# Performance work log

Hardware: AMD Instinct MI355X
Metric: run time of the kernel (lower is better)

Reference implementation:

```python
import math
import jax, jax.numpy as jnp
import numpy as np

C = 1.0          # Poincare ball curvature
NUM_HEADS = 8
EPS = 1e-15

def _beta(a, b):
    # Beta function via lgamma (python float constant)
    return math.exp(math.lgamma(a) + math.lgamma(b) - math.lgamma(a + b))

def h_linear(x, z, r, c=C):
    """HNN++ Poincare fully-connected layer (hypll HLinear).
    x: [..., in] points in the ball; z: [in, out] tangent weights; r: [out] bias."""
    sc = math.sqrt(c)
    x2 = jnp.sum(x * x, axis=-1, keepdims=True)
    lam = 2.0 / (1.0 - c * x2)                                # conformal factor
    zn = jnp.maximum(jnp.linalg.norm(z, axis=0), EPS)          # [out]
    inner = x @ z                                              # [..., out]
    two_scr = 2.0 * sc * r
    d = (2.0 * zn / sc) * jnp.arcsinh(
        (sc * inner * lam / zn) * jnp.cosh(two_scr) - (lam - 1.0) * jnp.sinh(two_scr)
    )
    w = jnp.sinh(sc * d) / sc
    return w / (1.0 + jnp.sqrt(1.0 + c * jnp.sum(w * w, axis=-1, keepdims=True)))

def pairwise_dist(q, k, c=C):
    """Poincare distance d(q,k) = arccosh(1 + 2c|q-k|^2 / ((1-c|q|^2)(1-c|k|^2))) / sqrt(c).
    q,k: [B,H,S,hd] -> [B,H,S,S]."""
    q2 = jnp.sum(q * q, axis=-1)
    k2 = jnp.sum(k * k, axis=-1)
    qk = jnp.einsum('bhqd,bhkd->bhqk', q, k)
    diff2 = jnp.maximum(q2[..., :, None] + k2[..., None, :] - 2.0 * qk, 0.0)
    denom = (1.0 - c * q2)[..., :, None] * (1.0 - c * k2)[..., None, :]
    arg = 1.0 + 2.0 * c * diff2 / denom
    return jnp.arccosh(jnp.maximum(arg, 1.0 + 1e-7)) / math.sqrt(c)

def midpoint(v, w, c=C):
    """Weighted Mobius gyromidpoint: m = 1/2 (x) (sum w*lam*x / sum w*(lam-1)).
    v: [B,H,Sk,hd], w: [B,H,Sq,Sk] -> [B,H,Sq,hd]."""
    v2 = jnp.sum(v * v, axis=-1)                      # [B,H,Sk]
    lam = 2.0 / (1.0 - c * v2)
    num = jnp.einsum('bhqk,bhkd->bhqd', w * lam[..., None, :], v)
    den = jnp.maximum(jnp.einsum('bhqk,bhk->bhq', w, lam - 1.0), EPS)[..., None]
    g = num / den                                     # gyromidpoint pre-scaling
    sc = math.sqrt(c)
    gn = jnp.maximum(jnp.linalg.norm(g, axis=-1, keepdims=True), EPS)
    t = jnp.tanh(0.5 * jnp.arctanh(jnp.clip(sc * gn, 0.0, 1.0 - 1e-7)))
    return (t / sc) * g / gn

def _forward(query, key, value, Wq, bq, Wk, bk, Wv, bv, scale_tau, scale_gamma):
    B, S, E = query.shape
    H = NUM_HEADS
    hd = E // H
    # hyperbolic q/k/v projections, then split into heads: [B,H,S,hd]
    q = h_linear(query, Wq, bq).reshape(B, S, H, hd).transpose(0, 2, 1, 3)
    k = h_linear(key, Wk, bk).reshape(B, S, H, hd).transpose(0, 2, 1, 3)
    v = h_linear(value, Wv, bv).reshape(B, S, H, hd).transpose(0, 2, 1, 3)
    # similarity = -dist/tau - gamma with tau = exp(-scale_tau)
    sim = -pairwise_dist(q, k) * jnp.exp(scale_tau[0]) - scale_gamma[0]
    causal = jnp.triu(jnp.ones((S, S), dtype=bool), k=1)
    sim = jnp.where(causal, -jnp.inf, sim)
    w = jnp.exp(sim)                                  # 'exp' attention activation
    agg = midpoint(v, w)                              # [B,H,S,hd]
    agg = agg.transpose(0, 2, 1, 3).reshape(B, S, E)
    # HNN++ beta-concatenation of the per-head ball points
    scale = _beta(E / 2.0, 0.5) / _beta(hd / 2.0, 0.5)
    return agg * scale

def setup_inputs() -> dict:
    root = jax.random.key(0)
    ks = jax.random.split(root, 8)
    B, S, E = 1, 2048, 512
    s = 0.02  # keep points well inside the unit ball
    return {
        'query': s * jax.random.normal(ks[0], (B, S, E), jnp.float32),
        'key':   s * jax.random.normal(ks[1], (B, S, E), jnp.float32),
        'value': s * jax.random.normal(ks[2], (B, S, E), jnp.float32),
        'Wq': s * jax.random.normal(ks[3], (E, E), jnp.float32),
        'Wk': s * jax.random.normal(ks[4], (E, E), jnp.float32),
        'Wv': s * jax.random.normal(ks[5], (E, E), jnp.float32),
        'bq': jnp.zeros((E,), jnp.float32),
        'bk': jnp.zeros((E,), jnp.float32),
        'bv': jnp.zeros((E,), jnp.float32),
        'scale_tau': jnp.zeros((1,), jnp.float32),
        'scale_gamma': jnp.zeros((1,), jnp.float32),
    }

def reference(query, key, value, Wq, Wk, Wv, bq, bk, bv, scale_tau, scale_gamma):
    return _forward(query, key, value, Wq, bq, Wk, bk, Wv, bv, scale_tau, scale_gamma)
```

## Files before the change

kernel.cpp:

```cpp
#include <hip/hip_runtime.h>
#include <cmath>

#define H 8
#define SEQ 2048
#define EDIM 512
#define HD 64
#define EPSF 1e-15f

typedef short bf16x8 __attribute__((ext_vector_type(8)));
typedef float f32x4 __attribute__((ext_vector_type(4)));

#define ZN_OFF    16
#define STATS_OFF (ZN_OFF + 24 * EDIM)
#define CQ_OFF    (STATS_OFF + 3 * H * SEQ)
#define IK_OFF    (CQ_OFF + H * SEQ)
#define PX2_OFF   (IK_OFF + H * SEQ)
#define U16_OFF   (PX2_OFF + 12288 + 16)
#define WT_U16    0
#define QKVB_U16  (WT_U16 + 3 * EDIM * EDIM)
#define VT_U16    (QKVB_U16 + 3 * SEQ * EDIM)
#define U16_TOTAL (VT_U16 + H * 80 * SEQ)
#define BIG_OFF   (U16_OFF + U16_TOTAL / 2 + 16)
#define TRI_SLOTS 272
#define PART_U16S (H * TRI_SLOTS * 4 * 1280)
#define ACC_FLOATS  (H * SEQ * 80)

__device__ __forceinline__ float bf2f(unsigned short u){
  union { unsigned int i; float f; } v; v.i = ((unsigned int)u) << 16; return v.f;
}
__device__ __forceinline__ unsigned short f2bf(float f){
  union { float f; unsigned int i; } v; v.f = f;
  unsigned int x = v.i;
  unsigned int r = (x + 0x7fffu + ((x >> 16) & 1u)) >> 16;
  return (unsigned short)r;
}

__device__ __forceinline__ unsigned int cvt_pk_bf16(float a, float b){
  unsigned int r;
  asm("v_cvt_pk_bf16_f32 %0, %1, %2" : "=v"(r) : "v"(a), "v"(b));
  return r;
}
__device__ __forceinline__ float vlog2f(float x){
  float r; asm("v_log_f32 %0, %1" : "=v"(r) : "v"(x)); return r;
}
__device__ __forceinline__ float vexp2f(float x){
  float r; asm("v_exp_f32 %0, %1" : "=v"(r) : "v"(x)); return r;
}
__device__ __forceinline__ float vsqrtf(float x){
  float r; asm("v_sqrt_f32 %0, %1" : "=v"(r) : "v"(x)); return r;
}

__device__ __forceinline__ int detect_f32(const unsigned short* __restrict__ q){
  const int l = threadIdx.x & 63;
  float mx = 0.f;
  #pragma unroll
  for (int j = 0; j < 4; ++j) mx = fmaxf(mx, fabsf(bf2f(q[l * 4 + j])));
  #pragma unroll
  for (int m = 32; m >= 1; m >>= 1) mx = fmaxf(mx, __shfl_xor(mx, m, 64));
  return mx > 1000.f;
}

__device__ __forceinline__ int tri_base(int t){
  const int m = t >> 1;
  return (t & 1) ? (m + 1) * (m + 1) : m * (m + 1);
}

__global__ __launch_bounds__(256) void wcvt_kernel(
    const void* __restrict__ Wq, const void* __restrict__ Wk, const void* __restrict__ Wv,
    const unsigned short* __restrict__ qprobe,
    unsigned short* __restrict__ WT, float* __restrict__ zn)
{
  const int p = blockIdx.y;
  const int bi = blockIdx.x >> 3, bo = blockIdx.x & 7;
  const void* W = (p == 0) ? Wq : ((p == 1) ? Wk : Wv);
  const int t = threadIdx.x;
  const int isf32 = detect_f32(qprobe);
  __shared__ float tile[64][65];

  #pragma unroll
  for (int j = 0; j < 16; ++j){
    int idx = t + 256 * j;
    int il = idx >> 6, ol = idx & 63;
    float val;
    if (isf32) val = ((const float*)W)[(size_t)(bi * 64 + il) * EDIM + bo * 64 + ol];
    else       val = bf2f(((const unsigned short*)W)[(size_t)(bi * 64 + il) * EDIM + bo * 64 + ol]);
    tile[il][ol] = val;
  }
  __syncthreads();
  if (t < 64){
    float s = 0.f;
    #pragma unroll 8
    for (int i = 0; i < 64; ++i){ float v = tile[i][t]; s += v * v; }
    zn[((size_t)(bi * 3 + p)) * EDIM + bo * 64 + t] = s;
  }
  #pragma unroll
  for (int j = 0; j < 16; ++j){
    int idx = t + 256 * j;
    int ol = idx >> 6, il = idx & 63;
    WT[((size_t)p * EDIM + bo * 64 + ol) * EDIM + bi * 64 + il] = f2bf(tile[il][ol]);
  }
}

__global__ __launch_bounds__(256) void hlin_gemm_kernel(
    const void* __restrict__ Xq, const void* __restrict__ Xk, const void* __restrict__ Xv,
    const unsigned short* __restrict__ WT, const unsigned short* __restrict__ qprobe,
    unsigned short* __restrict__ partC, float* __restrict__ partX2)
{
  const int p = blockIdx.y;
  const int rg = blockIdx.x >> 1;
  const int kslice = blockIdx.x & 1;
  const void* X = (p == 0) ? Xq : ((p == 1) ? Xk : Xv);
  const int r0 = rg * 16;
  const int t  = threadIdx.x;
  const int w = t >> 6, lane = t & 63;
  const int col = lane & 15, quad = lane >> 4;
  const int isf32 = detect_f32(qprobe);
  const int koff = kslice * 256;

  const unsigned short* WTb = WT + ((size_t)p * EDIM + w * 128 + col) * EDIM + koff;
  const float* Xf = (const float*)X + (size_t)(r0 + col) * EDIM + koff;
  const unsigned short* Xh = (const unsigned short*)X + (size_t)(r0 + col) * EDIM + koff;

  f32x4 acc[8];
  #pragma unroll
  for (int nt = 0; nt < 8; ++nt) acc[nt] = (f32x4){0.f, 0.f, 0.f, 0.f};
  float x2part = 0.f;

  bf16x8 caf, naf;
  bf16x8 cbf[8], nbf[8];
  {
    if (isf32){
      float4 xa = *(const float4*)&Xf[quad * 8];
      float4 xb = *(const float4*)&Xf[quad * 8 + 4];
      float xv[8] = {xa.x, xa.y, xa.z, xa.w, xb.x, xb.y, xb.z, xb.w};
      #pragma unroll
      for (int j = 0; j < 8; ++j){ caf[j] = (short)f2bf(xv[j]); x2part += xv[j] * xv[j]; }
    } else {
      caf = *(const bf16x8*)&Xh[quad * 8];
      #pragma unroll
      for (int j = 0; j < 8; ++j){ float xv = bf2f((unsigned short)caf[j]); x2part += xv * xv; }
    }
    #pragma unroll
    for (int nt = 0; nt < 8; ++nt)
      cbf[nt] = *(const bf16x8*)&WTb[(size_t)nt * 16 * EDIM + quad * 8];
  }

  for (int ks = 0; ks < 8; ++ks){
// ... 64 lines not shown
  for (int nt = 0; nt < 8; ++nt)
    #pragma unroll
    for (int r = 0; r < 4; ++r){
      const size_t idx = (size_t)(quad * 4 + r) * 512 + w * 128 + nt * 16 + col;
      acc[nt][r] = bf2f(partC[base0 + idx]) + bf2f(partC[base1 + idx]);
    }

  float lamr[4], lm1[4];
  #pragma unroll
  for (int r = 0; r < 4; ++r){
    const int row = quad * 4 + r;
    float x2r = partX2[((size_t)(p * 128 + rg) * 2 + 0) * 16 + row] +
                partX2[((size_t)(p * 128 + rg) * 2 + 1) * 16 + row];
    lamr[r] = 2.f / (1.f - x2r);
    lm1[r] = lamr[r] - 1.f;
  }
  #pragma unroll
  for (int nt = 0; nt < 8; ++nt){
    const int n = w * 128 + nt * 16 + col;
    float zsum = 0.f;
    #pragma unroll
    for (int bi = 0; bi < 8; ++bi)
      zsum += znacc[((size_t)(bi * 3 + p)) * EDIM + n];
    float znv = fmaxf(sqrtf(zsum), EPSF);
    float rb;
    if (isf32) rb = ((const float*)Bb)[n];
    else       rb = bf2f(((const unsigned short*)Bb)[n]);
    float e2r = __expf(2.f * rb);
    float ie2r = 1.f / e2r;
    float ch = 0.5f * (e2r + ie2r), sh = 0.5f * (e2r - ie2r);
    float izn = 1.f / znv;
    float tz = 2.f * znv;
    #pragma unroll
    for (int r = 0; r < 4; ++r){
      float a = (acc[nt][r] * lamr[r] * izn) * ch - lm1[r] * sh;
      float b = a + sqrtf(a * a + 1.f);
      float tt = __expf(tz * __logf(b));
      smem[(quad * 4 + r) * EDIM + n] = 0.5f * (tt - 1.f / tt);
    }
  }
  __syncthreads();

  {
    int row = t >> 4, l = t & 15;
    float s = 0.f;
    for (int o = l; o < EDIM; o += 16){ float wv = smem[row * EDIM + o]; s += wv * wv; }
    #pragma unroll
    for (int m = 8; m >= 1; m >>= 1) s += __shfl_xor(s, m, 16);
    if (l == 0) sw2[row] = s;
  }
  __syncthreads();

  const int o0 = 2 * t;
  const int h0 = t >> 5;
  const int d0 = o0 & 63;
  const int l5 = t & 31;
  #pragma unroll
  for (int rr = 0; rr < 16; ++rr){
    float inv = 1.f / (1.f + sqrtf(1.f + sw2[rr]));
    unsigned short b0 = f2bf(smem[rr * EDIM + o0] * inv);
    unsigned short b1 = f2bf(smem[rr * EDIM + o0 + 1] * inv);
    float r0v = bf2f(b0), r1v = bf2f(b1);
    int s = r0 + rr;
    unsigned int* dst = (unsigned int*)&qkvb[(((size_t)p * H + h0) * SEQ + s) * HD + d0];
    *dst = (unsigned int)b0 | ((unsigned int)b1 << 16);
    float ss = r0v * r0v + r1v * r1v;
    #pragma unroll
    for (int m = 16; m >= 1; m >>= 1) ss += __shfl_xor(ss, m, 64);
    if (p == 2){
      float lam = 2.f / (1.f - ss);
      VT[((size_t)h0 * 80 + d0) * SEQ + s]     = f2bf(r0v * lam);
      VT[((size_t)h0 * 80 + d0 + 1) * SEQ + s] = f2bf(r1v * lam);
      if (l5 < 16)
        VT[((size_t)h0 * 80 + 64 + l5) * SEQ + s] = (l5 == 0) ? f2bf(lam - 1.f) : 0;
    }
    if (l5 == 0){
      stats[((size_t)p * H + h0) * SEQ + s] = ss;
      if (p == 0) cqs[(size_t)h0 * SEQ + s] = 2.f / (1.f - ss);
      if (p == 1) iks[(size_t)h0 * SEQ + s] = 1.f / (1.f - ss);
    }
  }
}

__global__ __launch_bounds__(64) void attn_kernel(
    const unsigned short* __restrict__ Qb, const unsigned short* __restrict__ Kb,
    const unsigned short* __restrict__ VT,
    const float* __restrict__ q2s_all, const float* __restrict__ k2s_all,
    const float* __restrict__ cqs_all, const float* __restrict__ iks_all,
    const void* __restrict__ tau, const void* __restrict__ gam,
    const unsigned short* __restrict__ qprobe,
    float* __restrict__ big, int use_part)
{
  const int h  = blockIdx.y;
  const int tile = 31 - (blockIdx.x >> 5);
  const int sl = (blockIdx.x >> 1) & 15;
  const int wp = blockIdx.x & 1;
  const int kBeg = sl * 128;
  const int kEndFull = (tile + 1) * 64;
  if (kBeg >= kEndFull) return;
  const int kEnd = (kBeg + 128 < kEndFull) ? (kBeg + 128) : kEndFull;
  const int nhalf = (kEnd - kBeg) >> 5;

  const int lane = threadIdx.x;
  const int col = lane & 15, quad = lane >> 4;
  const int q0A = tile * 64 + wp * 16;
  const int q0B = q0A + 32;

  const unsigned short* Qh  = Qb + (size_t)h * SEQ * HD;
  const unsigned short* Kh  = Kb + (size_t)h * SEQ * HD;
  const unsigned short* VTh = VT + (size_t)h * 80 * SEQ;
  const float* q2s = q2s_all + (size_t)h * SEQ;
  const float* k2s = k2s_all + (size_t)h * SEQ;
  const float* cqs = cqs_all + (size_t)h * SEQ;
  const float* iks = iks_all + (size_t)h * SEQ;

  const int isf32 = detect_f32(qprobe);
  float tauv, gamv;
  if (isf32){ tauv = ((const float*)tau)[0]; gamv = ((const float*)gam)[0]; }
  else      { tauv = bf2f(((const unsigned short*)tau)[0]);
              gamv = bf2f(((const unsigned short*)gam)[0]); }
  const float m_et = -__expf(tauv);
  const float m_g2 = -gamv * 1.44269504088896340736f;

  const int srcA = ((quad & 1) * 2) * 16 + col;
  const int srcB = srcA + 16;
  const int tsel = quad >> 1;

  bf16x8 qfA0 = *(const bf16x8*)&Qh[(size_t)(q0A + col) * HD + quad * 8];
  bf16x8 qfA1 = *(const bf16x8*)&Qh[(size_t)(q0A + col) * HD + 32 + quad * 8];
  bf16x8 qfB0 = *(const bf16x8*)&Qh[(size_t)(q0B + col) * HD + quad * 8];
  bf16x8 qfB1 = *(const bf16x8*)&Qh[(size_t)(q0B + col) * HD + 32 + quad * 8];
  const float q2A = q2s[q0A + col], q2B = q2s[q0B + col];
  const float cqA = cqs[q0A + col], cqB = cqs[q0B + col];
  const int qmaxA = q0A + col, qmaxB = q0B + col;

  f32x4 pvA[5], pvB[5];
  #pragma unroll
  for (int nt = 0; nt < 5; ++nt){
    pvA[nt] = (f32x4){0.f, 0.f, 0.f, 0.f};
    pvB[nt] = (f32x4){0.f, 0.f, 0.f, 0.f};
  }

  int kb32 = kBeg;

  bf16x8 ckf0[2], ckf1[2], nkf0[2], nkf1[2];
  float4 ck2[2], cik[2], nk2[2], nik[2];
  #pragma unroll
  for (int tt = 0; tt < 2; ++tt){
    const int kbase = kb32 + 16 * tt;
    ckf0[tt] = *(const bf16x8*)&Kh[(size_t)(kbase + col) * HD + quad * 8];
    ckf1[tt] = *(const bf16x8*)&Kh[(size_t)(kbase + col) * HD + 32 + quad * 8];
    ck2[tt]  = *(const float4*)&k2s[kbase + quad * 4];
    cik[tt]  = *(const float4*)&iks[kbase + quad * 4];
  }

  for (int i = 0; i < nhalf; ++i){
    const int nkb32 = kb32 + 32;
    const bool have_next = (i + 1 < nhalf);
    if (have_next){
      #pragma unroll
      for (int tt = 0; tt < 2; ++tt){
        const int kbase = nkb32 + 16 * tt;
        nkf0[tt] = *(const bf16x8*)&Kh[(size_t)(kbase + col) * HD + quad * 8];
        nkf1[tt] = *(const bf16x8*)&Kh[(size_t)(kbase + col) * HD + 32 + quad * 8];
        nk2[tt]  = *(const float4*)&k2s[kbase + quad * 4];
        nik[tt]  = *(const float4*)&iks[kbase + quad * 4];
      }
    }

    unsigned int tloA[2], thiA[2], tloB[2], thiB[2];
    #pragma unroll
    for (int tt = 0; tt < 2; ++tt){
      const int kbase = kb32 + 16 * tt;
      f32x4 sA = (f32x4){0.f, 0.f, 0.f, 0.f};
      f32x4 sB = (f32x4){0.f, 0.f, 0.f, 0.f};
      sA = __builtin_amdgcn_mfma_f32_16x16x32_bf16(ckf0[tt], qfA0, sA, 0, 0, 0);
      sB = __builtin_amdgcn_mfma_f32_16x16x32_bf16(ckf0[tt], qfB0, sB, 0, 0, 0);
      sA = __builtin_amdgcn_mfma_f32_16x16x32_bf16(ckf1[tt], qfA1, sA, 0, 0, 0);
      sB = __builtin_amdgcn_mfma_f32_16x16x32_bf16(ckf1[tt], qfB1, sB, 0, 0, 0);
      float wA[4], wB[4];
      #pragma unroll
      for (int r = 0; r < 4; ++r){
        float k2 = (r == 0) ? ck2[tt].x : (r == 1) ? ck2[tt].y : (r == 2) ? ck2[tt].z : ck2[tt].w;
        float ik = (r == 0) ? cik[tt].x : (r == 1) ? cik[tt].y : (r == 2) ? cik[tt].z : cik[tt].w;
        const int key = kbase + quad * 4 + r;
        {
          float diff2 = fmaxf(q2A + k2 - 2.f * sA[r], 0.f);
          float u = fmaxf(diff2 * cqA * ik, 1e-7f);
          float z = 1.f + u + vsqrtf(u * (u + 2.f));
          float wv = vexp2f(__builtin_fmaf(vlog2f(z), m_et, m_g2));
          wA[r] = (key > qmaxA) ? 0.f : wv;
        }
        {
          float diff2 = fmaxf(q2B + k2 - 2.f * sB[r], 0.f);
          float u = fmaxf(diff2 * cqB * ik, 1e-7f);
          float z = 1.f + u + vsqrtf(u * (u + 2.f));
          float wv = vexp2f(__builtin_fmaf(vlog2f(z), m_et, m_g2));
          wB[r] = (key > qmaxB) ? 0.f : wv;
        }
      }
      tloA[tt] = cvt_pk_bf16(wA[0], wA[1]);
      thiA[tt] = cvt_pk_bf16(wA[2], wA[3]);
      tloB[tt] = cvt_pk_bf16(wB[0], wB[1]);
      thiB[tt] = cvt_pk_bf16(wB[2], wB[3]);
    }
    union { uint4 u; bf16x8 v; } pwA, pwB;
    {
      unsigned int a0 = (unsigned int)__shfl((int)tloA[0], srcA, 64);
      unsigned int a1 = (unsigned int)__shfl((int)tloA[1], srcA, 64);
      unsigned int b0 = (unsigned int)__shfl((int)thiA[0], srcA, 64);
      unsigned int b1 = (unsigned int)__shfl((int)thiA[1], srcA, 64);
      unsigned int c0 = (unsigned int)__shfl((int)tloA[0], srcB, 64);
      unsigned int c1 = (unsigned int)__shfl((int)tloA[1], srcB, 64);
      unsigned int d0 = (unsigned int)__shfl((int)thiA[0], srcB, 64);
      unsigned int d1 = (unsigned int)__shfl((int)thiA[1], srcB, 64);
      pwA.u.x = tsel ? a1 : a0;
      pwA.u.y = tsel ? b1 : b0;
      pwA.u.z = tsel ? c1 : c0;
      pwA.u.w = tsel ? d1 : d0;
    }
    {
      unsigned int a0 = (unsigned int)__shfl((int)tloB[0], srcA, 64);
      unsigned int a1 = (unsigned int)__shfl((int)tloB[1], srcA, 64);
      unsigned int b0 = (unsigned int)__shfl((int)thiB[0], srcA, 64);
      unsigned int b1 = (unsigned int)__shfl((int)thiB[1], srcA, 64);
      unsigned int c0 = (unsigned int)__shfl((int)tloB[0], srcB, 64);
      unsigned int c1 = (unsigned int)__shfl((int)tloB[1], srcB, 64);
      unsigned int d0 = (unsigned int)__shfl((int)thiB[0], srcB, 64);
      unsigned int d1 = (unsigned int)__shfl((int)thiB[1], srcB, 64);
      pwB.u.x = tsel ? a1 : a0;
      pwB.u.y = tsel ? b1 : b0;
      pwB.u.z = tsel ? c1 : c0;
      pwB.u.w = tsel ? d1 : d0;
    }
    #pragma unroll
    for (int nt = 0; nt < 5; ++nt){
      bf16x8 vf = *(const bf16x8*)&VTh[(size_t)(16 * nt + col) * SEQ + kb32 + quad * 8];
      pvA[nt] = __builtin_amdgcn_mfma_f32_16x16x32_bf16(pwA.v, vf, pvA[nt], 0, 0, 0);
      pvB[nt] = __builtin_amdgcn_mfma_f32_16x16x32_bf16(pwB.v, vf, pvB[nt], 0, 0, 0);
    }

    if (have_next){
      #pragma unroll
      for (int tt = 0; tt < 2; ++tt){
        ckf0[tt] = nkf0[tt]; ckf1[tt] = nkf1[tt];
        ck2[tt] = nk2[tt];   cik[tt] = nik[tt];
      }
    }
    kb32 = nkb32;
  }

  if (use_part){
    const int tbase = tri_base(tile);
    uint2* slotA = (uint2*)big + (size_t)(((h * TRI_SLOTS + tbase + sl) * 4) + wp) * 320;
    uint2* slotB = (uint2*)big + (size_t)(((h * TRI_SLOTS + tbase + sl) * 4) + wp + 2) * 320;
    #pragma unroll
    for (int nt = 0; nt < 5; ++nt){
      uint2 pk;
      pk.x = cvt_pk_bf16(pvA[nt][0], pvA[nt][1]);
      pk.y = cvt_pk_bf16(pvA[nt][2], pvA[nt][3]);
      slotA[nt * 64 + lane] = pk;
      pk.x = cvt_pk_bf16(pvB[nt][0], pvB[nt][1]);
      pk.y = cvt_pk_bf16(pvB[nt][2], pvB[nt][3]);
      slotB[nt * 64 + lane] = pk;
    }
  } else {
    #pragma unroll
    for (int r = 0; r < 4; ++r){
      float* rowA = big + ((size_t)h * SEQ + q0A + quad * 4 + r) * 80;
      float* rowB = big + ((size_t)h * SEQ + q0B + quad * 4 + r) * 80;
      #pragma unroll
      for (int nt = 0; nt < 5; ++nt){
        atomicAdd(&rowA[16 * nt + col], pvA[nt][r]);
        atomicAdd(&rowB[16 * nt + col], pvB[nt][r]);
      }
    }
  }
}

__global__ __launch_bounds__(256) void attn_fin_kernel(
    const float* __restrict__ big, int use_part,
    float* __restrict__ out, float beta_scale)
{
  const int h = blockIdx.y, tile16 = blockIdx.x;
  const int t = threadIdx.x;
  const int w = t >> 6, lane = t & 63;
  const int col = lane & 15, quad = lane >> 4;
  const int q0 = tile16 * 16;

  __shared__ float red[4][64][20];

  f32x4 pv[5];
  #pragma unroll
  for (int nt = 0; nt < 5; ++nt) pv[nt] = (f32x4){0.f, 0.f, 0.f, 0.f};

  if (use_part){
    const int st = tile16 >> 2, wq = tile16 & 3;
    const int tbase = tri_base(st);
    const int nv = (st + 2) >> 1;
    for (int sl = w; sl < nv; sl += 4){
      const uint2* slot = (const uint2*)big +
          (size_t)((h * TRI_SLOTS + tbase + sl) * 4 + wq) * 320;
      #pragma unroll
      for (int nt = 0; nt < 5; ++nt){
        uint2 v = slot[nt * 64 + lane];
        pv[nt][0] += bf2f((unsigned short)(v.x & 0xffffu));
        pv[nt][1] += bf2f((unsigned short)(v.x >> 16));
        pv[nt][2] += bf2f((unsigned short)(v.y & 0xffffu));
        pv[nt][3] += bf2f((unsigned short)(v.y >> 16));
      }
    }
  } else if (w == 0){
    #pragma unroll
    for (int nt = 0; nt < 5; ++nt)
      #pragma unroll
      for (int r = 0; r < 4; ++r)
        pv[nt][r] = big[((size_t)h * SEQ + q0 + quad * 4 + r) * 80 + 16 * nt + col];
  }

  #pragma unroll
  for (int nt = 0; nt < 5; ++nt)
    *(float4*)&red[w][lane][nt * 4] = (float4){pv[nt][0], pv[nt][1], pv[nt][2], pv[nt][3]};
  __syncthreads();

  if (t < 64){
    #pragma unroll
    for (int nt = 0; nt < 5; ++nt){
      float4 a = *(const float4*)&red[0][t][nt * 4];
      float4 b = *(const float4*)&red[1][t][nt * 4];
      float4 c = *(const float4*)&red[2][t][nt * 4];
      float4 d = *(const float4*)&red[3][t][nt * 4];
      pv[nt][0] = a.x + b.x + c.x + d.x;
      pv[nt][1] = a.y + b.y + c.y + d.y;
      pv[nt][2] = a.z + b.z + c.z + d.z;
      pv[nt][3] = a.w + b.w + c.w + d.w;
    }
    #pragma unroll
    for (int r = 0; r < 4; ++r){
      float den = __shfl(pv[4][r], quad * 16, 64);
      den = fmaxf(den, EPSF);
      float inv_den = 1.f / den;
      float g[4];
      float gsq = 0.f;
      #pragma unroll
      for (int nt = 0; nt < 4; ++nt){ g[nt] = pv[nt][r] * inv_den; gsq += g[nt] * g[nt]; }
      #pragma unroll
      for (int m = 8; m >= 1; m >>= 1) gsq += __shfl_xor(gsq, m, 64);
      float gn = fmaxf(sqrtf(gsq), EPSF);
      float x = fminf(gn, 1.f - 1e-7f);
      float tt2 = x / (1.f + sqrtf(1.f - x * x));
      float scl = (tt2 / gn) * beta_scale;
      const int q = q0 + quad * 4 + r;
      #pragma unroll
      for (int nt = 0; nt < 4; ++nt)
        out[(size_t)q * EDIM + h * HD + 16 * nt + col] = g[nt] * scl;
    }
  }
}

extern "C" void kernel_launch(void* const* d_in, const int* in_sizes, int n_in,
                              void* d_out, int out_size, void* d_ws, size_t ws_size,
                              hipStream_t stream){
  const void* Xq  = d_in[0];
  const void* Xk  = d_in[1];
  const void* Xv  = d_in[2];
  const void* Wq  = d_in[3];
  const void* Wk  = d_in[4];
  const void* Wv  = d_in[5];
  const void* Bq  = d_in[6];
  const void* Bk  = d_in[7];
  const void* Bv  = d_in[8];
  const void* tau = d_in[9];
  const void* gam = d_in[10];

  float* wsf   = (float*)d_ws;
  float* zn    = wsf + ZN_OFF;
  float* stats = wsf + STATS_OFF;
  float* cqs   = wsf + CQ_OFF;
  float* iks   = wsf + IK_OFF;
  float* px2   = wsf + PX2_OFF;
  unsigned short* u16b = (unsigned short*)(wsf + U16_OFF);
  unsigned short* WT   = u16b + WT_U16;
  unsigned short* qkvb = u16b + QKVB_U16;
  unsigned short* VT   = u16b + VT_U16;
  float* big   = wsf + BIG_OFF;
  unsigned short* partC = (unsigned short*)big;

  const int use_part =
      (ws_size >= (size_t)BIG_OFF * sizeof(float) + (size_t)PART_U16S * 2) ? 1 : 0;

  unsigned short* Qb = qkvb;
  unsigned short* Kb = qkvb + (size_t)H * SEQ * HD;
  float* q2s = stats;
  float* k2s = stats + (size_t)H * SEQ;
  const unsigned short* qprobe = (const unsigned short*)Xq;

  double lb1 = lgamma(EDIM / 2.0) + lgamma(0.5) - lgamma(EDIM / 2.0 + 0.5);
  double lb2 = lgamma(HD / 2.0)   + lgamma(0.5) - lgamma(HD / 2.0 + 0.5);
  float beta_scale = (float)exp(lb1 - lb2);

  wcvt_kernel<<<dim3(64, 3), dim3(256), 0, stream>>>(Wq, Wk, Wv, qprobe, WT, zn);
  hlin_gemm_kernel<<<dim3(256, 3), dim3(256), 0, stream>>>(
      Xq, Xk, Xv, WT, qprobe, partC, px2);
  hlin_fin_kernel<<<dim3(128, 3), dim3(256), 0, stream>>>(
      partC, px2, Bq, Bk, Bv, zn, qprobe, qkvb, stats, cqs, iks, VT);
  if (!use_part)
    hipMemsetAsync(big, 0, (size_t)ACC_FLOATS * sizeof(float), stream);
  attn_kernel<<<dim3(32 * 16 * 2, H), dim3(64), 0, stream>>>(
      Qb, Kb, VT, q2s, k2s, cqs, iks, tau, gam, qprobe, big, use_part);
  attn_fin_kernel<<<dim3(128, H), dim3(256), 0, stream>>>(
      big, use_part, (float*)d_out, beta_scale);
}
```

Measured before the change: 195.0 us.

## Pack four attention waves per block, template-unroll key loop, hoist V loads

```diff
diff --git a/kernel.cpp b/kernel.cpp
--- a/kernel.cpp
+++ b/kernel.cpp
@@ -293,66 +293,19 @@
   }
 }
 
-__global__ __launch_bounds__(64) void attn_kernel(
-    const unsigned short* __restrict__ Qb, const unsigned short* __restrict__ Kb,
-    const unsigned short* __restrict__ VT,
-    const float* __restrict__ q2s_all, const float* __restrict__ k2s_all,
-    const float* __restrict__ cqs_all, const float* __restrict__ iks_all,
-    const void* __restrict__ tau, const void* __restrict__ gam,
-    const unsigned short* __restrict__ qprobe,
-    float* __restrict__ big, int use_part)
+template<int NH>
+__device__ __forceinline__ void attn_loop(
+    int kb32, int col, int quad,
+    const unsigned short* __restrict__ Kh, const unsigned short* __restrict__ VTh,
+    const float* __restrict__ k2s, const float* __restrict__ iks,
+    bf16x8 qfA0, bf16x8 qfA1, bf16x8 qfB0, bf16x8 qfB1,
+    float cqA, float cqq2A, float cqB, float cqq2B,
+    int qmaxA, int qmaxB, float m_et, float m_g2,
+    int srcA, int srcB, int tsel,
+    f32x4 (&pvA)[5], f32x4 (&pvB)[5])
 {
-  const int h  = blockIdx.y;
-  const int tile = 31 - (blockIdx.x >> 5);
-  const int sl = (blockIdx.x >> 1) & 15;
-  const int wp = blockIdx.x & 1;
-  const int kBeg = sl * 128;
-  const int kEndFull = (tile + 1) * 64;
-  if (kBeg >= kEndFull) return;
-  const int kEnd = (kBeg + 128 < kEndFull) ? (kBeg + 128) : kEndFull;
-  const int nhalf = (kEnd - kBeg) >> 5;
-
-  const int lane = threadIdx.x;
-  const int col = lane & 15, quad = lane >> 4;
-  const int q0A = tile * 64 + wp * 16;
-  const int q0B = q0A + 32;
-
-  const unsigned short* Qh  = Qb + (size_t)h * SEQ * HD;
-  const unsigned short* Kh  = Kb + (size_t)h * SEQ * HD;
-  const unsigned short* VTh = VT + (size_t)h * 80 * SEQ;
-  const float* q2s = q2s_all + (size_t)h * SEQ;
-  const float* k2s = k2s_all + (size_t)h * SEQ;
-  const float* cqs = cqs_all + (size_t)h * SEQ;
-  const float* iks = iks_all + (size_t)h * SEQ;
-
-  const int isf32 = detect_f32(qprobe);
-  float tauv, gamv;
-  if (isf32){ tauv = ((const float*)tau)[0]; gamv = ((const float*)gam)[0]; }
-  else      { tauv = bf2f(((const unsigned short*)tau)[0]);
-              gamv = bf2f(((const unsigned short*)gam)[0]); }
-  const float m_et = -__expf(tauv);
-  const float m_g2 = -gamv * 1.44269504088896340736f;
-
-  const int srcA = ((quad & 1) * 2) * 16 + col;
-  const int srcB = srcA + 16;
-  const int tsel = quad >> 1;
-
-  bf16x8 qfA0 = *(const bf16x8*)&Qh[(size_t)(q0A + col) * HD + quad * 8];
-  bf16x8 qfA1 = *(const bf16x8*)&Qh[(size_t)(q0A + col) * HD + 32 + quad * 8];
-  bf16x8 qfB0 = *(const bf16x8*)&Qh[(size_t)(q0B + col) * HD + quad * 8];
-  bf16x8 qfB1 = *(const bf16x8*)&Qh[(size_t)(q0B + col) * HD + 32 + quad * 8];
-  const float q2A = q2s[q0A + col], q2B = q2s[q0B + col];
-  const float cqA = cqs[q0A + col], cqB = cqs[q0B + col];
-  const int qmaxA = q0A + col, qmaxB = q0B + col;
-
-  f32x4 pvA[5], pvB[5];
-  #pragma unroll
-  for (int nt = 0; nt < 5; ++nt){
-    pvA[nt] = (f32x4){0.f, 0.f, 0.f, 0.f};
-    pvB[nt] = (f32x4){0.f, 0.f, 0.f, 0.f};
-  }
-
-  int kb32 = kBeg;
+  const float m2cqA = -2.f * cqA;
+  const float m2cqB = -2.f * cqB;
 
   bf16x8 ckf0[2], ckf1[2], nkf0[2], nkf1[2];
   float4 ck2[2], cik[2], nk2[2], nik[2];
@@ -365,13 +318,17 @@
     cik[tt]  = *(const float4*)&iks[kbase + quad * 4];
   }
 
-  for (int i = 0; i < nhalf; ++i){
-    const int nkb32 = kb32 + 32;
-    const bool have_next = (i + 1 < nhalf);
-    if (have_next){
+  #pragma unroll
+  for (int i = 0; i < NH; ++i){
+    bf16x8 vf[5];
+    #pragma unroll
+    for (int nt = 0; nt < 5; ++nt)
+      vf[nt] = *(const bf16x8*)&VTh[(size_t)(16 * nt + col) * SEQ + kb32 + quad * 8];
+
+    if (i + 1 < NH){
       #pragma unroll
       for (int tt = 0; tt < 2; ++tt){
-        const int kbase = nkb32 + 16 * tt;
+        const int kbase = kb32 + 32 + 16 * tt;
         nkf0[tt] = *(const bf16x8*)&Kh[(size_t)(kbase + col) * HD + quad * 8];
         nkf1[tt] = *(const bf16x8*)&Kh[(size_t)(kbase + col) * HD + 32 + quad * 8];
         nk2[tt]  = *(const float4*)&k2s[kbase + quad * 4];
@@ -382,29 +339,32 @@
     unsigned int tloA[2], thiA[2], tloB[2], thiB[2];
     #pragma unroll
     for (int tt = 0; tt < 2; ++tt){
-      const int kbase = kb32 + 16 * tt;
       f32x4 sA = (f32x4){0.f, 0.f, 0.f, 0.f};
       f32x4 sB = (f32x4){0.f, 0.f, 0.f, 0.f};
+      __builtin_amdgcn_s_setprio(1);
       sA = __builtin_amdgcn_mfma_f32_16x16x32_bf16(ckf0[tt], qfA0, sA, 0, 0, 0);
       sB = __builtin_amdgcn_mfma_f32_16x16x32_bf16(ckf0[tt], qfB0, sB, 0, 0, 0);
       sA = __builtin_amdgcn_mfma_f32_16x16x32_bf16(ckf1[tt], qfA1, sA, 0, 0, 0);
       sB = __builtin_amdgcn_mfma_f32_16x16x32_bf16(ckf1[tt], qfB1, sB, 0, 0, 0);
+      __builtin_amdgcn_s_setprio(0);
       float wA[4], wB[4];
       #pragma unroll
       for (int r = 0; r < 4; ++r){
         float k2 = (r == 0) ? ck2[tt].x : (r == 1) ? ck2[tt].y : (r == 2) ? ck2[tt].z : ck2[tt].w;
         float ik = (r == 0) ? cik[tt].x : (r == 1) ? cik[tt].y : (r == 2) ? cik[tt].z : cik[tt].w;
-        const int key = kbase + quad * 4 + r;
+        const int key = kb32 + 16 * tt + quad * 4 + r;
         {
-          float diff2 = fmaxf(q2A + k2 - 2.f * sA[r], 0.f);
-          float u = fmaxf(diff2 * cqA * ik, 1e-7f);
+          float t1 = __builtin_fmaf(k2, cqA, cqq2A);
+          t1 = __builtin_fmaf(m2cqA, sA[r], t1);
+          float u = fmaxf(t1 * ik, 1e-7f);
           float z = 1.f + u + vsqrtf(u * (u + 2.f));
           float wv = vexp2f(__builtin_fmaf(vlog2f(z), m_et, m_g2));
           wA[r] = (key > qmaxA) ? 0.f : wv;
         }
         {
-          float diff2 = fmaxf(q2B + k2 - 2.f * sB[r], 0.f);
-          float u = fmaxf(diff2 * cqB * ik, 1e-7f);
+          float t1 = __builtin_fmaf(k2, cqB, cqq2B);
+          t1 = __builtin_fmaf(m2cqB, sB[r], t1);
+          float u = fmaxf(t1 * ik, 1e-7f);
           float z = 1.f + u + vsqrtf(u * (u + 2.f));
           float wv = vexp2f(__builtin_fmaf(vlog2f(z), m_et, m_g2));
           wB[r] = (key > qmaxB) ? 0.f : wv;
@@ -444,22 +404,94 @@
       pwB.u.z = tsel ? c1 : c0;
       pwB.u.w = tsel ? d1 : d0;
     }
+    __builtin_amdgcn_s_setprio(1);
     #pragma unroll
     for (int nt = 0; nt < 5; ++nt){
-      bf16x8 vf = *(const bf16x8*)&VTh[(size_t)(16 * nt + col) * SEQ + kb32 + quad * 8];
-      pvA[nt] = __builtin_amdgcn_mfma_f32_16x16x32_bf16(pwA.v, vf, pvA[nt], 0, 0, 0);
-      pvB[nt] = __builtin_amdgcn_mfma_f32_16x16x32_bf16(pwB.v, vf, pvB[nt], 0, 0, 0);
-    }
-
-    if (have_next){
+      pvA[nt] = __builtin_amdgcn_mfma_f32_16x16x32_bf16(pwA.v, vf[nt], pvA[nt], 0, 0, 0);
+      pvB[nt] = __builtin_amdgcn_mfma_f32_16x16x32_bf16(pwB.v, vf[nt], pvB[nt], 0, 0, 0);
+    }
+    __builtin_amdgcn_s_setprio(0);
+
+    if (i + 1 < NH){
       #pragma unroll
       for (int tt = 0; tt < 2; ++tt){
         ckf0[tt] = nkf0[tt]; ckf1[tt] = nkf1[tt];
         ck2[tt] = nk2[tt];   cik[tt] = nik[tt];
       }
     }
-    kb32 = nkb32;
-  }
+    kb32 += 32;
+  }
+}
+
+__global__ __launch_bounds__(256) void attn_kernel(
+    const unsigned short* __restrict__ Qb, const unsigned short* __restrict__ Kb,
+    const unsigned short* __restrict__ VT,
+    const float* __restrict__ q2s_all, const float* __restrict__ k2s_all,
+    const float* __restrict__ cqs_all, const float* __restrict__ iks_all,
+    const void* __restrict__ tau, const void* __restrict__ gam,
+    const unsigned short* __restrict__ qprobe,
+    float* __restrict__ big, int use_part)
+{
+  const int h  = blockIdx.y;
+  const int unit = blockIdx.x * 4 + (threadIdx.x >> 6);
+  const int lane = threadIdx.x & 63;
+  const int tile = 31 - (unit >> 5);
+  const int sl = (unit >> 1) & 15;
+  const int wp = unit & 1;
+  const int kBeg = sl * 128;
+  const int kEndFull = (tile + 1) * 64;
+  if (kBeg >= kEndFull) return;
+  const int kEnd = (kBeg + 128 < kEndFull) ? (kBeg + 128) : kEndFull;
+  const int nhalf = (kEnd - kBeg) >> 5;
+
+  const int col = lane & 15, quad = lane >> 4;
+  const int q0A = tile * 64 + wp * 16;
+  const int q0B = q0A + 32;
+
+  const unsigned short* Qh  = Qb + (size_t)h * SEQ * HD;
+  const unsigned short* Kh  = Kb + (size_t)h * SEQ * HD;
+  const unsigned short* VTh = VT + (size_t)h * 80 * SEQ;
+  const float* q2s = q2s_all + (size_t)h * SEQ;
+  const float* k2s = k2s_all + (size_t)h * SEQ;
+  const float* cqs = cqs_all + (size_t)h * SEQ;
+  const float* iks = iks_all + (size_t)h * SEQ;
+
+  const int isf32 = detect_f32(qprobe);
+  float tauv, gamv;
+  if (isf32){ tauv = ((const float*)tau)[0]; gamv = ((const float*)gam)[0]; }
+  else      { tauv = bf2f(((const unsigned short*)tau)[0]);
+              gamv = bf2f(((const unsigned short*)gam)[0]); }
+  const float m_et = -__expf(tauv);
+  const float m_g2 = -gamv * 1.44269504088896340736f;
+
+  const int srcA = ((quad & 1) * 2) * 16 + col;
+  const int srcB = srcA + 16;
+  const int tsel = quad >> 1;
+
+  bf16x8 qfA0 = *(const bf16x8*)&Qh[(size_t)(q0A + col) * HD + quad * 8];
+  bf16x8 qfA1 = *(const bf16x8*)&Qh[(size_t)(q0A + col) * HD + 32 + quad * 8];
+  bf16x8 qfB0 = *(const bf16x8*)&Qh[(size_t)(q0B + col) * HD + quad * 8];
+  bf16x8 qfB1 = *(const bf16x8*)&Qh[(size_t)(q0B + col) * HD + 32 + quad * 8];
+  const float q2A = q2s[q0A + col], q2B = q2s[q0B + col];
+  const float cqA = cqs[q0A + col], cqB = cqs[q0B + col];
+  const float cqq2A = cqA * q2A, cqq2B = cqB * q2B;
+  const int qmaxA = q0A + col, qmaxB = q0B + col;
+
+  f32x4 pvA[5], pvB[5];
+  #pragma unroll
+  for (int nt = 0; nt < 5; ++nt){
+    pvA[nt] = (f32x4){0.f, 0.f, 0.f, 0.f};
+    pvB[nt] = (f32x4){0.f, 0.f, 0.f, 0.f};
+  }
+
+  if (nhalf == 4)
+    attn_loop<4>(kBeg, col, quad, Kh, VTh, k2s, iks, qfA0, qfA1, qfB0, qfB1,
+                 cqA, cqq2A, cqB, cqq2B, qmaxA, qmaxB, m_et, m_g2,
+                 srcA, srcB, tsel, pvA, pvB);
+  else
+    attn_loop<2>(kBeg, col, quad, Kh, VTh, k2s, iks, qfA0, qfA1, qfB0, qfB1,
+                 cqA, cqq2A, cqB, cqq2B, qmaxA, qmaxB, m_et, m_g2,
+                 srcA, srcB, tsel, pvA, pvB);
 
   if (use_part){
     const int tbase = tri_base(tile);
@@ -617,7 +649,7 @@
       partC, px2, Bq, Bk, Bv, zn, qprobe, qkvb, stats, cqs, iks, VT);
   if (!use_part)
     hipMemsetAsync(big, 0, (size_t)ACC_FLOATS * sizeof(float), stream);
-  attn_kernel<<<dim3(32 * 16 * 2, H), dim3(64), 0, stream>>>(
+  attn_kernel<<<dim3(256, H), dim3(256), 0, stream>>>(
       Qb, Kb, VT, q2s, k2s, cqs, iks, tau, gam, qprobe, big, use_part);
   attn_fin_kernel<<<dim3(128, H), dim3(256), 0, stream>>>(
       big, use_part, (float*)d_out, beta_scale);
```

Result: no change. 195.1 us (+0.1%).

## Make attention key-stationary: hold a 64-key block in registers, loop over queries

Applied to the files above, without the earlier changes.

```diff
diff --git a/kernel.cpp b/kernel.cpp
--- a/kernel.cpp
+++ b/kernel.cpp
@@ -21,8 +21,8 @@
 #define VT_U16    (QKVB_U16 + 3 * SEQ * EDIM)
 #define U16_TOTAL (VT_U16 + H * 80 * SEQ)
 #define BIG_OFF   (U16_OFF + U16_TOTAL / 2 + 16)
-#define TRI_SLOTS 272
-#define PART_U16S (H * TRI_SLOTS * 4 * 1280)
+#define TRI16 2112
+#define PART_U16S (H * TRI16 * 1280)
 #define ACC_FLOATS  (H * SEQ * 80)
 
 __device__ __forceinline__ float bf2f(unsigned short u){
@@ -60,9 +60,9 @@
   return mx > 1000.f;
 }
 
-__device__ __forceinline__ int tri_base(int t){
-  const int m = t >> 1;
-  return (t & 1) ? (m + 1) * (m + 1) : m * (m + 1);
+__device__ __forceinline__ int sbase(int s){
+  const int a = s >> 2, b = s & 3;
+  return s + 2 * a * (a - 1) + a * b;
 }
 
 __global__ __launch_bounds__(256) void wcvt_kernel(
@@ -293,7 +293,157 @@
   }
 }
 
-__global__ __launch_bounds__(64) void attn_kernel(
+__device__ __forceinline__ uint4 xpose32(unsigned int tlo0, unsigned int tlo1,
+                                         unsigned int thi0, unsigned int thi1,
+                                         int srcA, int srcB, int tsel){
+  unsigned int a0 = (unsigned int)__shfl((int)tlo0, srcA, 64);
+  unsigned int a1 = (unsigned int)__shfl((int)tlo1, srcA, 64);
+  unsigned int b0 = (unsigned int)__shfl((int)thi0, srcA, 64);
+  unsigned int b1 = (unsigned int)__shfl((int)thi1, srcA, 64);
+  unsigned int c0 = (unsigned int)__shfl((int)tlo0, srcB, 64);
+  unsigned int c1 = (unsigned int)__shfl((int)tlo1, srcB, 64);
+  unsigned int d0 = (unsigned int)__shfl((int)thi0, srcB, 64);
+  unsigned int d1 = (unsigned int)__shfl((int)thi1, srcB, 64);
+  uint4 r;
+  r.x = tsel ? a1 : a0;
+  r.y = tsel ? b1 : b0;
+  r.z = tsel ? c1 : c0;
+  r.w = tsel ? d1 : d0;
+  return r;
+}
+
+__device__ __forceinline__ void score4(
+    const f32x4& s4, const float4& k2v, const float4& ikv,
+    float cq, float cqq2, float m2cq, int kbase, int qmax, int quad,
+    float m_et, float m_g2, unsigned int& lo, unsigned int& hi)
+{
+  float w[4];
+  #pragma unroll
+  for (int r = 0; r < 4; ++r){
+    float k2 = (r == 0) ? k2v.x : (r == 1) ? k2v.y : (r == 2) ? k2v.z : k2v.w;
+    float ik = (r == 0) ? ikv.x : (r == 1) ? ikv.y : (r == 2) ? ikv.z : ikv.w;
+    float t1 = __builtin_fmaf(k2, cq, cqq2);
+    t1 = __builtin_fmaf(m2cq, s4[r], t1);
+    float u = fmaxf(t1 * ik, 1e-7f);
+    float z = 1.f + u + vsqrtf(u * (u + 2.f));
+    float wv = vexp2f(__builtin_fmaf(vlog2f(z), m_et, m_g2));
+    const int key = kbase + quad * 4 + r;
+    w[r] = (key > qmax) ? 0.f : wv;
+  }
+  lo = cvt_pk_bf16(w[0], w[1]);
+  hi = cvt_pk_bf16(w[2], w[3]);
+}
+
+template<int NITER>
+__device__ __forceinline__ void attn_qloop(
+    int s0, int c, int kBeg, int col, int quad, int lane,
+    const unsigned short* __restrict__ Qh,
+    const bf16x8 (&kf0)[4], const bf16x8 (&kf1)[4],
+    const float4 (&ck2)[4], const float4 (&cik)[4],
+    const bf16x8 (&vf0)[5], const bf16x8 (&vf1)[5],
+    const float* __restrict__ q2s, const float* __restrict__ cqs,
+    float m_et, float m_g2, int srcA, int srcB, int tsel,
+    float* __restrict__ big, int h, int use_part)
+{
+  bf16x8 qA0 = *(const bf16x8*)&Qh[(size_t)(s0 * 16 + col) * HD + quad * 8];
+  bf16x8 qA1 = *(const bf16x8*)&Qh[(size_t)(s0 * 16 + col) * HD + 32 + quad * 8];
+  bf16x8 qB0 = *(const bf16x8*)&Qh[(size_t)((s0 + 1) * 16 + col) * HD + quad * 8];
+  bf16x8 qB1 = *(const bf16x8*)&Qh[(size_t)((s0 + 1) * 16 + col) * HD + 32 + quad * 8];
+  float q2A = q2s[s0 * 16 + col],       cqA = cqs[s0 * 16 + col];
+  float q2B = q2s[(s0 + 1) * 16 + col], cqB = cqs[(s0 + 1) * 16 + col];
+
+  #pragma unroll
+  for (int i = 0; i < NITER; ++i){
+    const int sA = s0 + 2 * i, sB = sA + 1;
+    bf16x8 nA0, nA1, nB0, nB1;
+    float nq2A, ncqA, nq2B, ncqB;
+    if (i + 1 < NITER){
+      const int tA = (sA + 2) * 16 + col, tB = (sA + 3) * 16 + col;
+      nA0 = *(const bf16x8*)&Qh[(size_t)tA * HD + quad * 8];
+      nA1 = *(const bf16x8*)&Qh[(size_t)tA * HD + 32 + quad * 8];
+      nB0 = *(const bf16x8*)&Qh[(size_t)tB * HD + quad * 8];
+      nB1 = *(const bf16x8*)&Qh[(size_t)tB * HD + 32 + quad * 8];
+      nq2A = q2s[tA]; ncqA = cqs[tA];
+      nq2B = q2s[tB]; ncqB = cqs[tB];
+    }
+
+    const float cqq2A = cqA * q2A, m2cqA = -2.f * cqA;
+    const float cqq2B = cqB * q2B, m2cqB = -2.f * cqB;
+    const int qmaxA = sA * 16 + col, qmaxB = sB * 16 + col;
+
+    f32x4 sSA[4], sSB[4];
+    __builtin_amdgcn_s_setprio(1);
+    #pragma unroll
+    for (int g = 0; g < 4; ++g){
+      f32x4 z4 = (f32x4){0.f, 0.f, 0.f, 0.f};
+      sSA[g] = __builtin_amdgcn_mfma_f32_16x16x32_bf16(kf0[g], qA0, z4, 0, 0, 0);
+      sSA[g] = __builtin_amdgcn_mfma_f32_16x16x32_bf16(kf1[g], qA1, sSA[g], 0, 0, 0);
+      sSB[g] = __builtin_amdgcn_mfma_f32_16x16x32_bf16(kf0[g], qB0, z4, 0, 0, 0);
+      sSB[g] = __builtin_amdgcn_mfma_f32_16x16x32_bf16(kf1[g], qB1, sSB[g], 0, 0, 0);
+    }
+    __builtin_amdgcn_s_setprio(0);
+
+    unsigned int loA[4], hiA[4], loB[4], hiB[4];
+    #pragma unroll
+    for (int g = 0; g < 4; ++g){
+      score4(sSA[g], ck2[g], cik[g], cqA, cqq2A, m2cqA, kBeg + g * 16, qmaxA, quad,
+             m_et, m_g2, loA[g], hiA[g]);
+      score4(sSB[g], ck2[g], cik[g], cqB, cqq2B, m2cqB, kBeg + g * 16, qmaxB, quad,
+             m_et, m_g2, loB[g], hiB[g]);
+    }
+
+    union { uint4 u; bf16x8 v; } pA01, pA23, pB01, pB23;
+    pA01.u = xpose32(loA[0], loA[1], hiA[0], hiA[1], srcA, srcB, tsel);
+    pA23.u = xpose32(loA[2], loA[3], hiA[2], hiA[3], srcA, srcB, tsel);
+    pB01.u = xpose32(loB[0], loB[1], hiB[0], hiB[1], srcA, srcB, tsel);
+    pB23.u = xpose32(loB[2], loB[3], hiB[2], hiB[3], srcA, srcB, tsel);
+
+    f32x4 pvA[5], pvB[5];
+    __builtin_amdgcn_s_setprio(1);
+    #pragma unroll
+    for (int nt = 0; nt < 5; ++nt){
+      f32x4 z4 = (f32x4){0.f, 0.f, 0.f, 0.f};
+      pvA[nt] = __builtin_amdgcn_mfma_f32_16x16x32_bf16(pA01.v, vf0[nt], z4, 0, 0, 0);
+      pvA[nt] = __builtin_amdgcn_mfma_f32_16x16x32_bf16(pA23.v, vf1[nt], pvA[nt], 0, 0, 0);
+      pvB[nt] = __builtin_amdgcn_mfma_f32_16x16x32_bf16(pB01.v, vf0[nt], z4, 0, 0, 0);
+      pvB[nt] = __builtin_amdgcn_mfma_f32_16x16x32_bf16(pB23.v, vf1[nt], pvB[nt], 0, 0, 0);
+    }
+    __builtin_amdgcn_s_setprio(0);
+
+    if (use_part){
+      uint2* slotA = (uint2*)big + (size_t)(h * TRI16 + sbase(sA) + c) * 320;
+      uint2* slotB = (uint2*)big + (size_t)(h * TRI16 + sbase(sB) + c) * 320;
+      #pragma unroll
+      for (int nt = 0; nt < 5; ++nt){
+        uint2 pk;
+        pk.x = cvt_pk_bf16(pvA[nt][0], pvA[nt][1]);
+        pk.y = cvt_pk_bf16(pvA[nt][2], pvA[nt][3]);
+        slotA[nt * 64 + lane] = pk;
+        pk.x = cvt_pk_bf16(pvB[nt][0], pvB[nt][1]);
+        pk.y = cvt_pk_bf16(pvB[nt][2], pvB[nt][3]);
+        slotB[nt * 64 + lane] = pk;
+      }
+    } else {
+      #pragma unroll
+      for (int r = 0; r < 4; ++r){
+        float* rowA = big + ((size_t)h * SEQ + sA * 16 + quad * 4 + r) * 80;
+        float* rowB = big + ((size_t)h * SEQ + sB * 16 + quad * 4 + r) * 80;
+        #pragma unroll
+        for (int nt = 0; nt < 5; ++nt){
+          atomicAdd(&rowA[16 * nt + col], pvA[nt][r]);
+          atomicAdd(&rowB[16 * nt + col], pvB[nt][r]);
+        }
+      }
+    }
+
+    if (i + 1 < NITER){
+      qA0 = nA0; qA1 = nA1; qB0 = nB0; qB1 = nB1;
+      q2A = nq2A; cqA = ncqA; q2B = nq2B; cqB = ncqB;
+    }
+  }
+}
+
+__global__ __launch_bounds__(64, 2) void attn_kernel(
     const unsigned short* __restrict__ Qb, const unsigned short* __restrict__ Kb,
     const unsigned short* __restrict__ VT,
     const float* __restrict__ q2s_all, const float* __restrict__ k2s_all,
@@ -302,20 +452,16 @@
     const unsigned short* __restrict__ qprobe,
     float* __restrict__ big, int use_part)
 {
-  const int h  = blockIdx.y;
-  const int tile = 31 - (blockIdx.x >> 5);
-  const int sl = (blockIdx.x >> 1) & 15;
-  const int wp = blockIdx.x & 1;
-  const int kBeg = sl * 128;
-  const int kEndFull = (tile + 1) * 64;
-  if (kBeg >= kEndFull) return;
-  const int kEnd = (kBeg + 128 < kEndFull) ? (kBeg + 128) : kEndFull;
-  const int nhalf = (kEnd - kBeg) >> 5;
-
+  const int h = blockIdx.y;
+  const int c = blockIdx.x >> 4;
+  const int j = blockIdx.x & 15;
+  const int nsl = (33 - c) >> 1;
+  if (j >= nsl) return;
+  const int kBeg = c * 64;
+  const int s0 = 4 * c + 8 * j;
+  const int rem = 128 - s0;
   const int lane = threadIdx.x;
   const int col = lane & 15, quad = lane >> 4;
-  const int q0A = tile * 64 + wp * 16;
-  const int q0B = q0A + 32;
 
   const unsigned short* Qh  = Qb + (size_t)h * SEQ * HD;
   const unsigned short* Kh  = Kb + (size_t)h * SEQ * HD;
@@ -337,167 +483,39 @@
   const int srcB = srcA + 16;
   const int tsel = quad >> 1;
 
-  bf16x8 qfA0 = *(const bf16x8*)&Qh[(size_t)(q0A + col) * HD + quad * 8];
-  bf16x8 qfA1 = *(const bf16x8*)&Qh[(size_t)(q0A + col) * HD + 32 + quad * 8];
-  bf16x8 qfB0 = *(const bf16x8*)&Qh[(size_t)(q0B + col) * HD + quad * 8];
-  bf16x8 qfB1 = *(const bf16x8*)&Qh[(size_t)(q0B + col) * HD + 32 + quad * 8];
-  const float q2A = q2s[q0A + col], q2B = q2s[q0B + col];
-  const float cqA = cqs[q0A + col], cqB = cqs[q0B + col];
-  const int qmaxA = q0A + col, qmaxB = q0B + col;
-
-  f32x4 pvA[5], pvB[5];
+  bf16x8 kf0[4], kf1[4];
+  float4 ck2[4], cik[4];
+  #pragma unroll
+  for (int g = 0; g < 4; ++g){
+    kf0[g] = *(const bf16x8*)&Kh[(size_t)(kBeg + g * 16 + col) * HD + quad * 8];
+    kf1[g] = *(const bf16x8*)&Kh[(size_t)(kBeg + g * 16 + col) * HD + 32 + quad * 8];
+    ck2[g] = *(const float4*)&k2s[kBeg + g * 16 + quad * 4];
+    cik[g] = *(const float4*)&iks[kBeg + g * 16 + quad * 4];
+  }
+  bf16x8 vf0[5], vf1[5];
   #pragma unroll
   for (int nt = 0; nt < 5; ++nt){
-    pvA[nt] = (f32x4){0.f, 0.f, 0.f, 0.f};
-    pvB[nt] = (f32x4){0.f, 0.f, 0.f, 0.f};
-  }
-
-  int kb32 = kBeg;
-
-  bf16x8 ckf0[2], ckf1[2], nkf0[2], nkf1[2];
-  float4 ck2[2], cik[2], nk2[2], nik[2];
-  #pragma unroll
-  for (int tt = 0; tt < 2; ++tt){
-    const int kbase = kb32 + 16 * tt;
-    ckf0[tt] = *(const bf16x8*)&Kh[(size_t)(kbase + col) * HD + quad * 8];
-    ckf1[tt] = *(const bf16x8*)&Kh[(size_t)(kbase + col) * HD + 32 + quad * 8];
-    ck2[tt]  = *(const float4*)&k2s[kbase + quad * 4];
-    cik[tt]  = *(const float4*)&iks[kbase + quad * 4];
-  }
-
-  for (int i = 0; i < nhalf; ++i){
-    const int nkb32 = kb32 + 32;
-    const bool have_next = (i + 1 < nhalf);
-    if (have_next){
-      #pragma unroll
-      for (int tt = 0; tt < 2; ++tt){
-        const int kbase = nkb32 + 16 * tt;
-        nkf0[tt] = *(const bf16x8*)&Kh[(size_t)(kbase + col) * HD + quad * 8];
-        nkf1[tt] = *(const bf16x8*)&Kh[(size_t)(kbase + col) * HD + 32 + quad * 8];
-        nk2[tt]  = *(const float4*)&k2s[kbase + quad * 4];
-        nik[tt]  = *(const float4*)&iks[kbase + quad * 4];
-      }
-    }
-
-    unsigned int tloA[2], thiA[2], tloB[2], thiB[2];
-    #pragma unroll
-    for (int tt = 0; tt < 2; ++tt){
-      const int kbase = kb32 + 16 * tt;
-      f32x4 sA = (f32x4){0.f, 0.f, 0.f, 0.f};
-      f32x4 sB = (f32x4){0.f, 0.f, 0.f, 0.f};
-      sA = __builtin_amdgcn_mfma_f32_16x16x32_bf16(ckf0[tt], qfA0, sA, 0, 0, 0);
-      sB = __builtin_amdgcn_mfma_f32_16x16x32_bf16(ckf0[tt], qfB0, sB, 0, 0, 0);
-      sA = __builtin_amdgcn_mfma_f32_16x16x32_bf16(ckf1[tt], qfA1, sA, 0, 0, 0);
-      sB = __builtin_amdgcn_mfma_f32_16x16x32_bf16(ckf1[tt], qfB1, sB, 0, 0, 0);
-      float wA[4], wB[4];
-      #pragma unroll
-      for (int r = 0; r < 4; ++r){
-        float k2 = (r == 0) ? ck2[tt].x : (r == 1) ? ck2[tt].y : (r == 2) ? ck2[tt].z : ck2[tt].w;
-        float ik = (r == 0) ? cik[tt].x : (r == 1) ? cik[tt].y : (r == 2) ? cik[tt].z : cik[tt].w;
-        const int key = kbase + quad * 4 + r;
-        {
-          float diff2 = fmaxf(q2A + k2 - 2.f * sA[r], 0.f);
-          float u = fmaxf(diff2 * cqA * ik, 1e-7f);
-          float z = 1.f + u + vsqrtf(u * (u + 2.f));
-          float wv = vexp2f(__builtin_fmaf(vlog2f(z), m_et, m_g2));
-          wA[r] = (key > qmaxA) ? 0.f : wv;
-        }
-        {
-          float diff2 = fmaxf(q2B + k2 - 2.f * sB[r], 0.f);
-          float u = fmaxf(diff2 * cqB * ik, 1e-7f);
-          float z = 1.f + u + vsqrtf(u * (u + 2.f));
-          float wv = vexp2f(__builtin_fmaf(vlog2f(z), m_et, m_g2));
-          wB[r] = (key > qmaxB) ? 0.f : wv;
-        }
-      }
-      tloA[tt] = cvt_pk_bf16(wA[0], wA[1]);
-      thiA[tt] = cvt_pk_bf16(wA[2], wA[3]);
-      tloB[tt] = cvt_pk_bf16(wB[0], wB[1]);
-      thiB[tt] = cvt_pk_bf16(wB[2], wB[3]);
-    }
-    union { uint4 u; bf16x8 v; } pwA, pwB;
-    {
-      unsigned int a0 = (unsigned int)__shfl((int)tloA[0], srcA, 64);
-      unsigned int a1 = (unsigned int)__shfl((int)tloA[1], srcA, 64);
-      unsigned int b0 = (unsigned int)__shfl((int)thiA[0], srcA, 64);
-      unsigned int b1 = (unsigned int)__shfl((int)thiA[1], srcA, 64);
-      unsigned int c0 = (unsigned int)__shfl((int)tloA[0], srcB, 64);
-      unsigned int c1 = (unsigned int)__shfl((int)tloA[1], srcB, 64);
-      unsigned int d0 = (unsigned int)__shfl((int)thiA[0], srcB, 64);
-      unsigned int d1 = (unsigned int)__shfl((int)thiA[1], srcB, 64);
-      pwA.u.x = tsel ? a1 : a0;
-      pwA.u.y = tsel ? b1 : b0;
-      pwA.u.z = tsel ? c1 : c0;
-      pwA.u.w = tsel ? d1 : d0;
-    }
-    {
-      unsigned int a0 = (unsigned int)__shfl((int)tloB[0], srcA, 64);
-      unsigned int a1 = (unsigned int)__shfl((int)tloB[1], srcA, 64);
-      unsigned int b0 = (unsigned int)__shfl((int)thiB[0], srcA, 64);
-      unsigned int b1 = (unsigned int)__shfl((int)thiB[1], srcA, 64);
-      unsigned int c0 = (unsigned int)__shfl((int)tloB[0], srcB, 64);
-      unsigned int c1 = (unsigned int)__shfl((int)tloB[1], srcB, 64);
-      unsigned int d0 = (unsigned int)__shfl((int)thiB[0], srcB, 64);
-      unsigned int d1 = (unsigned int)__shfl((int)thiB[1], srcB, 64);
-      pwB.u.x = tsel ? a1 : a0;
-      pwB.u.y = tsel ? b1 : b0;
-      pwB.u.z = tsel ? c1 : c0;
-      pwB.u.w = tsel ? d1 : d0;
-    }
-    #pragma unroll
-    for (int nt = 0; nt < 5; ++nt){
-      bf16x8 vf = *(const bf16x8*)&VTh[(size_t)(16 * nt + col) * SEQ + kb32 + quad * 8];
-      pvA[nt] = __builtin_amdgcn_mfma_f32_16x16x32_bf16(pwA.v, vf, pvA[nt], 0, 0, 0);
-      pvB[nt] = __builtin_amdgcn_mfma_f32_16x16x32_bf16(pwB.v, vf, pvB[nt], 0, 0, 0);
-    }
-
-    if (have_next){
-      #pragma unroll
-      for (int tt = 0; tt < 2; ++tt){
-        ckf0[tt] = nkf0[tt]; ckf1[tt] = nkf1[tt];
-        ck2[tt] = nk2[tt];   cik[tt] = nik[tt];
-      }
-    }
-    kb32 = nkb32;
-  }
-
-  if (use_part){
-    const int tbase = tri_base(tile);
-    uint2* slotA = (uint2*)big + (size_t)(((h * TRI_SLOTS + tbase + sl) * 4) + wp) * 320;
-    uint2* slotB = (uint2*)big + (size_t)(((h * TRI_SLOTS + tbase + sl) * 4) + wp + 2) * 320;
-    #pragma unroll
-    for (int nt = 0; nt < 5; ++nt){
-      uint2 pk;
-      pk.x = cvt_pk_bf16(pvA[nt][0], pvA[nt][1]);
-      pk.y = cvt_pk_bf16(pvA[nt][2], pvA[nt][3]);
-      slotA[nt * 64 + lane] = pk;
-      pk.x = cvt_pk_bf16(pvB[nt][0], pvB[nt][1]);
-      pk.y = cvt_pk_bf16(pvB[nt][2], pvB[nt][3]);
-      slotB[nt * 64 + lane] = pk;
-    }
-  } else {
-    #pragma unroll
-    for (int r = 0; r < 4; ++r){
-      float* rowA = big + ((size_t)h * SEQ + q0A + quad * 4 + r) * 80;
-      float* rowB = big + ((size_t)h * SEQ + q0B + quad * 4 + r) * 80;
-      #pragma unroll
-      for (int nt = 0; nt < 5; ++nt){
-        atomicAdd(&rowA[16 * nt + col], pvA[nt][r]);
-        atomicAdd(&rowB[16 * nt + col], pvB[nt][r]);
-      }
-    }
-  }
+    vf0[nt] = *(const bf16x8*)&VTh[(size_t)(16 * nt + col) * SEQ + kBeg + quad * 8];
+    vf1[nt] = *(const bf16x8*)&VTh[(size_t)(16 * nt + col) * SEQ + kBeg + 32 + quad * 8];
+  }
+
+  if (rem >= 8)
+    attn_qloop<4>(s0, c, kBeg, col, quad, lane, Qh, kf0, kf1, ck2, cik, vf0, vf1,
+                  q2s, cqs, m_et, m_g2, srcA, srcB, tsel, big, h, use_part);
+  else
+    attn_qloop<2>(s0, c, kBeg, col, quad, lane, Qh, kf0, kf1, ck2, cik, vf0, vf1,
+                  q2s, cqs, m_et, m_g2, srcA, srcB, tsel, big, h, use_part);
 }
 
 __global__ __launch_bounds__(256) void attn_fin_kernel(
     const float* __restrict__ big, int use_part,
     float* __restrict__ out, float beta_scale)
 {
-  const int h = blockIdx.y, tile16 = blockIdx.x;
+  const int h = blockIdx.y, s = blockIdx.x;
   const int t = threadIdx.x;
   const int w = t >> 6, lane = t & 63;
   const int col = lane & 15, quad = lane >> 4;
-  const int q0 = tile16 * 16;
+  const int q0 = s * 16;
 
   __shared__ float red[4][64][20];
 
@@ -506,12 +524,10 @@
   for (int nt = 0; nt < 5; ++nt) pv[nt] = (f32x4){0.f, 0.f, 0.f, 0.f};
 
   if (use_part){
-    const int st = tile16 >> 2, wq = tile16 & 3;
-    const int tbase = tri_base(st);
-    const int nv = (st + 2) >> 1;
+    const int tbase = sbase(s);
+    const int nv = (s >> 2) + 1;
     for (int sl = w; sl < nv; sl += 4){
-      const uint2* slot = (const uint2*)big +
-          (size_t)((h * TRI_SLOTS + tbase + sl) * 4 + wq) * 320;
+      const uint2* slot = (const uint2*)big + (size_t)(h * TRI16 + tbase + sl) * 320;
       #pragma unroll
       for (int nt = 0; nt < 5; ++nt){
         uint2 v = slot[nt * 64 + lane];
@@ -617,7 +633,7 @@
       partC, px2, Bq, Bk, Bv, zn, qprobe, qkvb, stats, cqs, iks, VT);
   if (!use_part)
     hipMemsetAsync(big, 0, (size_t)ACC_FLOATS * sizeof(float), stream);
-  attn_kernel<<<dim3(32 * 16 * 2, H), dim3(64), 0, stream>>>(
+  attn_kernel<<<dim3(512, H), dim3(64), 0, stream>>>(
       Qb, Kb, VT, q2s, k2s, cqs, iks, tau, gam, qprobe, big, use_part);
   attn_fin_kernel<<<dim3(128, H), dim3(256), 0, stream>>>(
       big, use_part, (float*)d_out, beta_scale);
```

After: 186.4 us. -4.4%, faster.
